# Performance work log

Measured on AMD Instinct MI355X. Metric: run time of the kernel, lower is better.

Reference implementation:

```python
import jax, jax.numpy as jnp
import numpy as np

B, R, CIN, J, O, ITERS = 512, 1152, 8, 10, 16, 3  # batch, routes, in_ch, capsules, out_ch, routing iters


def squash(s, axis):
    # v = (||s||^2 / (1 + ||s||^2)) * s / ||s||  (standard CapsNet squash)
    sq = jnp.sum(s * s, axis=axis, keepdims=True)
    return (sq / (1.0 + sq)) * s * jax.lax.rsqrt(sq + 1e-8)


def setup_inputs() -> dict:
    key = jax.random.key(0)
    k1, k2 = jax.random.split(key)
    x = jax.random.normal(k1, (B, R, CIN), dtype=jnp.float32)
    W = jax.random.normal(k2, (R, J, O, CIN), dtype=jnp.float32)  # param, batch-broadcast
    return {"x": x, "W": W}


def reference(x, W):
    # u_hat[b,r,j,:] = W[r,j] @ x[b,r]   (replaces torch stack/cat broadcasting)
    u_hat = jnp.einsum('rjoc,brc->brjo', W, x)  # [B,R,J,O]
    b_ij = jnp.zeros((x.shape[0], R, J), dtype=x.dtype)
    v = None
    for it in range(ITERS):
        c_ij = jax.nn.softmax(b_ij, axis=2)                 # softmax over capsules j
        s_j = jnp.einsum('brj,brjo->bjo', c_ij, u_hat)      # weighted sum over routes
        v = squash(s_j, axis=-1)                            # [B,J,O]
        if it < ITERS - 1:
            b_ij = b_ij + jnp.einsum('brjo,bjo->brj', u_hat, v)  # agreement
    # torch returns v_j.squeeze(1) with shape [B, J, O, 1]
    return v[..., None]
```

## Files before the change

kernel.cpp:

```cpp
#include <hip/hip_runtime.h>
#include <hip/hip_fp16.h>
#include <cstdint>
#include <cstddef>

#define NB 512
#define NR 1152
#define NC 8
#define NJ 10
#define NO 16
#define NJO 160

typedef unsigned int uint32;

union H2U { __half2 h; uint32 u; };

__device__ __forceinline__ uint32 packf16(float a0, float a1) {
    H2U p;
    p.h = __halves2half2(__float2half_rn(a0), __float2half_rn(a1));
    return p.u;
}
__device__ __forceinline__ float2 unpackf16(uint32 w) {
    H2U p; p.u = w;
    return __half22float2(p.h);
}

__global__ __launch_bounds__(256) void xpose_kernel(const float* __restrict__ x,
                                                    float* __restrict__ xT) {
    const int r0 = blockIdx.x * 16;
    const int b0 = blockIdx.y * 64;
    const int t  = threadIdx.x;
    __shared__ float tile[16][65][8];

    for (int i = t; i < 2048; i += 256) {
        int b = i >> 5, r = (i >> 1) & 15, h = i & 1;
        float4 v = *(const float4*)&x[(size_t)(b0 + b) * (NR * NC) + (size_t)(r0 + r) * NC + h * 4];
        *(float4*)&tile[r][b][h * 4] = v;
    }
    __syncthreads();
    for (int i = t; i < 2048; i += 256) {
        int r = i >> 7, b = (i >> 1) & 63, h = i & 1;
        float4 v = *(const float4*)&tile[r][b][h * 4];
        *(float4*)&xT[(size_t)(r0 + r) * (NB * NC) + (size_t)(b0 + b) * NC + h * 4] = v;
    }
}

__global__ __launch_bounds__(320) void uhat_kernel(const float* __restrict__ xT,
                                                   const float* __restrict__ W,
                                                   uint32* __restrict__ u) {
    const int r = blockIdx.x;
    const int t = threadIdx.x;

    __shared__ float Ws[NC][NJO + 4];
    __shared__ float xs[NB][NC];

    for (int i = t; i < NJO * NC; i += 320) {
        Ws[i & 7][i >> 3] = W[(size_t)r * (NJO * NC) + i];
    }
    {
        const float4* xsrc = (const float4*)(xT + (size_t)r * (NB * NC));
        float4* xdst = (float4*)&xs[0][0];
        for (int i = t; i < (NB * NC) / 4; i += 320) xdst[i] = xsrc[i];
    }
    __syncthreads();

    const int ni   = t % 80;
    const int half = t / 80;
    const int g    = ni / 10;
    const int rem  = ni % 10;
    const int qt   = g >> 1;
    const int jh   = g & 1;
    const int j    = jh * 5 + (rem >> 1);
    const int d    = rem & 1;
    const int jo0  = 16 * j + 4 * qt + 2 * d;

    float w0[8], w1[8];
#pragma unroll
    for (int c = 0; c < 8; ++c) {
        w0[c] = Ws[c][jo0];
        w1[c] = Ws[c][jo0 + 1];
    }

    for (int b = half; b < NB; b += 4) {
        const float4* xp = (const float4*)xs[b];
        float4 xa = xp[0], xb = xp[1];
        float a0 = w0[0] * xa.x + w0[1] * xa.y + w0[2] * xa.z + w0[3] * xa.w
                 + w0[4] * xb.x + w0[5] * xb.y + w0[6] * xb.z + w0[7] * xb.w;
        float a1 = w1[0] * xa.x + w1[1] * xa.y + w1[2] * xa.z + w1[3] * xa.w
                 + w1[4] * xb.x + w1[5] * xb.y + w1[6] * xb.z + w1[7] * xb.w;
        u[(size_t)(b * NR + r) * 80 + ni] = packf16(a0, a1);
    }
}

#define LOADROW(Q0, Q1, Q2, Q3, Q4, ROW)                                      \
    {                                                                         \
        const uint32* p_ = ubase + (size_t)(ROW) * 80;                        \
        Q0 = *(const uint2*)(p_);     Q1 = *(const uint2*)(p_ + 2);           \
        Q2 = *(const uint2*)(p_ + 4); Q3 = *(const uint2*)(p_ + 6);           \
        Q4 = *(const uint2*)(p_ + 8);                                         \
    }

#define PROCESS(Q0, Q1, Q2, Q3, Q4)                                           \
    {                                                                         \
        uint32 ur[10];                                                        \
        ur[0] = Q0.x; ur[1] = Q0.y; ur[2] = Q1.x; ur[3] = Q1.y;               \
        ur[4] = Q2.x; ur[5] = Q2.y; ur[6] = Q3.x; ur[7] = Q3.y;               \
        ur[8] = Q4.x; ur[9] = Q4.y;                                           \
        float cj[5];                                                          \
        if (it == 0) {                                                        \
            _Pragma("unroll")                                                 \
            for (int jl = 0; jl < 5; ++jl) cj[jl] = 0.1f;                     \
        } else {                                                              \
            float sum = 0.0f;                                                 \
            _Pragma("unroll")                                                 \
            for (int jl = 0; jl < 5; ++jl) {                                  \
                float2 ua = unpackf16(ur[2 * jl]);                            \
                float2 ub = unpackf16(ur[2 * jl + 1]);                        \
                float4 vv = *(const float4*)&vls[vbase + 16 * jl];            \
                float pj = ua.x * vv.x + ua.y * vv.y + ub.x * vv.z + ub.y * vv.w; \
                pj += __shfl_xor(pj, 1);                                      \
                pj += __shfl_xor(pj, 2);                                      \
                float e = __expf(pj);                                         \
                cj[jl] = e;                                                   \
                sum += e;                                                     \
            }                                                                 \
            sum += __shfl_xor(sum, 4);                                        \
            float inv = 1.0f / sum;                                           \
            _Pragma("unroll")                                                 \
            for (int jl = 0; jl < 5; ++jl) cj[jl] *= inv;                     \
        }                                                                     \
        _Pragma("unroll")                                                     \
        for (int jl = 0; jl < 5; ++jl) {                                      \
            float2 ua = unpackf16(ur[2 * jl]);                                \
            float2 ub = unpackf16(ur[2 * jl + 1]);                            \
            acc[4 * jl + 0] += cj[jl] * ua.x;                                 \
            acc[4 * jl + 1] += cj[jl] * ua.y;                                 \
            acc[4 * jl + 2] += cj[jl] * ub.x;                                 \
            acc[4 * jl + 3] += cj[jl] * ub.y;                                 \
        }                                                                     \
    }

__global__ __launch_bounds__(576, 2) void routing_kernel(const uint32* __restrict__ u,
                                                         float* __restrict__ outp) {
    const int b    = blockIdx.x;
    const int t    = threadIdx.x;
    const int w    = t >> 6;
    const int l    = t & 63;
    const int qt   = l & 3;
    const int jh   = (l >> 2) & 1;
    const int mloc = l >> 3;
    const int g    = qt * 2 + jh;

    __shared__ float sl[NJO];
    __shared__ float vls[NJO];
    __shared__ float vaccl[NJO];

    for (int i = t; i < NJO; i += 576) sl[i] = 0.0f;
    __syncthreads();

    const uint32* ubase = u + (size_t)b * (NR * 80) + g * 10;
    const int vbase = jh * 80 + qt * 4;
    const int rbase = w * 128 + mloc;

#pragma unroll 1
    for (int it = 0; it < 3; ++it) {
        float acc[20];
#pragma unroll
        for (int i = 0; i < 20; ++i) acc[i] = 0.0f;

        uint2 qa0, qa1, qa2, qa3, qa4;
        uint2 qb0, qb1, qb2, qb3, qb4;

        LOADROW(qa0, qa1, qa2, qa3, qa4, rbase)

#pragma unroll 1
        for (int c16 = 0; c16 < 16; c16 += 2) {
            LOADROW(qb0, qb1, qb2, qb3, qb4, rbase + (c16 + 1) * 8)
            PROCESS(qa0, qa1, qa2, qa3, qa4)
            if (c16 < 14) {
                LOADROW(qa0, qa1, qa2, qa3, qa4, rbase + (c16 + 2) * 8)
            }
            PROCESS(qb0, qb1, qb2, qb3, qb4)
        }

        float a[12];
        {
            const int bit = (l >> 3) & 1;
#pragma unroll
            for (int i = 0; i < 12; ++i) {
                float lo = acc[i];
                float hi = (i + 12 < 20) ? acc[i + 12] : 0.0f;
                float send = bit ? lo : hi;
                float recv = __shfl_xor(send, 8);
                a[i] = (bit ? hi : lo) + recv;
            }
        }
#pragma unroll
        for (int st = 1; st < 3; ++st) {
            const int h = 12 >> st;
            const int bit = (l >> (3 + st)) & 1;
#pragma unroll
            for (int i = 0; i < 6; ++i) {
                if (i < h) {
                    float send = bit ? a[i] : a[i + h];
                    float recv = __shfl_xor(send, 8 << st);
                    a[i] = (bit ? a[i + h] : a[i]) + recv;
                }
            }
        }
        const int base = 3 * (__brev((uint32)mloc) >> 29);
#pragma unroll
        for (int i = 0; i < 3; ++i) {
            int aidx = base + i;
            if (aidx < 20) {
                int jl = aidx >> 2, e = aidx & 3;
                atomicAdd(&sl[16 * (jh * 5 + jl) + 4 * qt + e], a[i]);
            }
        }
        __syncthreads();

        if (t < 80) {
            float2 sv = *(const float2*)&sl[2 * t];
            float sq = sv.x * sv.x + sv.y * sv.y;
#pragma unroll
            for (int off = 1; off < 8; off <<= 1) sq += __shfl_xor(sq, off, 8);
            float scale = (sq / (1.0f + sq)) * rsqrtf(sq + 1e-8f);
            float vx = sv.x * scale, vy = sv.y * scale;
            if (it == 2) {
                *(float2*)&outp[b * NJO + 2 * t] = make_float2(vx, vy);
            } else {
                float2 va;
                if (it == 0) va = make_float2(vx, vy);
                else {
                    va = *(const float2*)&vaccl[2 * t];
                    va.x += vx; va.y += vy;
                }
                *(float2*)&vaccl[2 * t] = va;
                *(float2*)&vls[2 * t]   = va;
            }
        }
        __syncthreads();
        if (it < 2) {
            for (int i = t; i < NJO; i += 576) sl[i] = 0.0f;
            __syncthreads();
        }
    }
}

extern "C" void kernel_launch(void* const* d_in, const int* in_sizes, int n_in,
                              void* d_out, int out_size, void* d_ws, size_t ws_size,
                              hipStream_t stream) {
    (void)in_sizes; (void)n_in; (void)out_size; (void)ws_size;

    const float* x = (const float*)d_in[0];
    const float* W = (const float*)d_in[1];
    float* out = (float*)d_out;

    char* ws = (char*)d_ws;
    const size_t XBYTES = (size_t)NR * NB * NC * 4;
    float*  xT = (float*)ws;
    uint32* u  = (uint32*)(ws + XBYTES);

    xpose_kernel<<<dim3(NR / 16, NB / 64), 256, 0, stream>>>(x, xT);
    uhat_kernel<<<NR, 320, 0, stream>>>(xT, W, u);
    routing_kernel<<<NB, 576, 0, stream>>>(u, out);
}
```

Baseline: 212.6 us.

## Compute first routing iteration via fp32 GEMM, skip it in routing pass

Because the first routing iteration uses uniform coefficients, s_j is 0.1 times the sum over routes of u_hat, which equals W summed against x. A separate fp32 GEMM-like kernel computes this with atomics into a zeroed buffer that reuses the xT workspace. The routing kernel then starts at iteration 1, saving one full streaming pass over the fp16 u_hat tensor. It adds a memset, an extra kernel launch and global atomics.

```diff
diff --git a/kernel.cpp b/kernel.cpp
--- a/kernel.cpp
+++ b/kernel.cpp
@@ -22,6 +22,11 @@
 __device__ __forceinline__ float2 unpackf16(uint32 w) {
     H2U p; p.u = w;
     return __half22float2(p.h);
+}
+
+__device__ __forceinline__ float dot8f(float4 p, float4 q, float4 xa, float4 xb) {
+    return p.x * xa.x + p.y * xa.y + p.z * xa.z + p.w * xa.w
+         + q.x * xb.x + q.y * xb.y + q.z * xb.z + q.w * xb.w;
 }
 
 __global__ __launch_bounds__(256) void xpose_kernel(const float* __restrict__ x,
@@ -91,6 +96,51 @@
     }
 }
 
+__global__ __launch_bounds__(320) void s0gemm_kernel(const float* __restrict__ x,
+                                                     const float* __restrict__ W,
+                                                     float* __restrict__ s0) {
+    const int b0 = blockIdx.x * 32;
+    const int r0 = blockIdx.y * 32;
+    const int t  = threadIdx.x;
+
+    __shared__ float xs[32][32][8];
+
+    for (int i = t; i < 2048; i += 320) {
+        int bloc = i >> 6, rloc = (i >> 1) & 31, h = i & 1;
+        float4 v = *(const float4*)&x[(size_t)(b0 + bloc) * (NR * NC) + (size_t)(r0 + rloc) * NC + h * 4];
+        *(float4*)&xs[rloc][bloc][h * 4] = v;
+    }
+    __syncthreads();
+
+    const int jo = t % 160;
+    const int bh = t / 160;
+
+    const float* wp = W + (size_t)r0 * (NJO * NC) + (size_t)jo * NC;
+
+    float acc[16];
+#pragma unroll
+    for (int i = 0; i < 16; ++i) acc[i] = 0.0f;
+
+#pragma unroll 1
+    for (int rloc = 0; rloc < 32; ++rloc) {
+        const float* wr = wp + (size_t)rloc * (NJO * NC);
+        float4 w0 = *(const float4*)wr;
+        float4 w1 = *(const float4*)(wr + 4);
+#pragma unroll
+        for (int bs = 0; bs < 16; ++bs) {
+            const float* xp = xs[rloc][bh * 16 + bs];
+            float4 xa = *(const float4*)xp;
+            float4 xb = *(const float4*)(xp + 4);
+            acc[bs] += dot8f(w0, w1, xa, xb);
+        }
+    }
+
+#pragma unroll
+    for (int bs = 0; bs < 16; ++bs) {
+        atomicAdd(&s0[(size_t)(b0 + bh * 16 + bs) * NJO + jo], acc[bs]);
+    }
+}
+
 #define LOADROW(Q0, Q1, Q2, Q3, Q4, ROW)                                      \
     {                                                                         \
         const uint32* p_ = ubase + (size_t)(ROW) * 80;                        \
@@ -106,10 +156,7 @@
         ur[4] = Q2.x; ur[5] = Q2.y; ur[6] = Q3.x; ur[7] = Q3.y;               \
         ur[8] = Q4.x; ur[9] = Q4.y;                                           \
         float cj[5];                                                          \
-        if (it == 0) {                                                        \
-            _Pragma("unroll")                                                 \
-            for (int jl = 0; jl < 5; ++jl) cj[jl] = 0.1f;                     \
-        } else {                                                              \
+        {                                                                     \
             float sum = 0.0f;                                                 \
             _Pragma("unroll")                                                 \
             for (int jl = 0; jl < 5; ++jl) {                                  \
@@ -140,6 +187,7 @@
     }
 
 __global__ __launch_bounds__(576, 2) void routing_kernel(const uint32* __restrict__ u,
+                                                         const float* __restrict__ s0,
                                                          float* __restrict__ outp) {
     const int b    = blockIdx.x;
     const int t    = threadIdx.x;
@@ -155,6 +203,18 @@
     __shared__ float vaccl[NJO];
 
     for (int i = t; i < NJO; i += 576) sl[i] = 0.0f;
+
+    if (t < 80) {
+        float2 sv = *(const float2*)&s0[(size_t)b * NJO + 2 * t];
+        sv.x *= 0.1f; sv.y *= 0.1f;
+        float sq = sv.x * sv.x + sv.y * sv.y;
+#pragma unroll
+        for (int off = 1; off < 8; off <<= 1) sq += __shfl_xor(sq, off, 8);
+        float scale = (sq / (1.0f + sq)) * rsqrtf(sq + 1e-8f);
+        float vx = sv.x * scale, vy = sv.y * scale;
+        *(float2*)&vaccl[2 * t] = make_float2(vx, vy);
+        *(float2*)&vls[2 * t]   = make_float2(vx, vy);
+    }
     __syncthreads();
 
     const uint32* ubase = u + (size_t)b * (NR * 80) + g * 10;
@@ -162,7 +222,7 @@
     const int rbase = w * 128 + mloc;
 
 #pragma unroll 1
-    for (int it = 0; it < 3; ++it) {
+    for (int it = 1; it < 3; ++it) {
         float acc[20];
 #pragma unroll
         for (int i = 0; i < 20; ++i) acc[i] = 0.0f;
@@ -228,12 +288,8 @@
             if (it == 2) {
                 *(float2*)&outp[b * NJO + 2 * t] = make_float2(vx, vy);
             } else {
-                float2 va;
-                if (it == 0) va = make_float2(vx, vy);
-                else {
-                    va = *(const float2*)&vaccl[2 * t];
-                    va.x += vx; va.y += vy;
-                }
+                float2 va = *(const float2*)&vaccl[2 * t];
+                va.x += vx; va.y += vy;
                 *(float2*)&vaccl[2 * t] = va;
                 *(float2*)&vls[2 * t]   = va;
             }
@@ -256,11 +312,15 @@
     float* out = (float*)d_out;
 
     char* ws = (char*)d_ws;
-    const size_t XBYTES = (size_t)NR * NB * NC * 4;
+    const size_t XBYTES  = (size_t)NR * NB * NC * 4;
+    const size_t S0BYTES = (size_t)NB * NJO * 4;
     float*  xT = (float*)ws;
     uint32* u  = (uint32*)(ws + XBYTES);
+    float*  s0 = (float*)ws;
 
     xpose_kernel<<<dim3(NR / 16, NB / 64), 256, 0, stream>>>(x, xT);
     uhat_kernel<<<NR, 320, 0, stream>>>(xT, W, u);
-    routing_kernel<<<NB, 576, 0, stream>>>(u, out);
-}
+    hipMemsetAsync(s0, 0, S0BYTES, stream);
+    s0gemm_kernel<<<dim3(16, 36), 320, 0, stream>>>(x, W, s0);
+    routing_kernel<<<NB, 576, 0, stream>>>(u, s0, out);
+}
```

Measured after the change: 243.0 us. 14.3% more time.
